# Kernel optimization log

Measured on AMD Instinct MI355X. Metric: run time of the kernel, lower is better.

Reference implementation:

```python
import jax, jax.numpy as jnp
import numpy as np

K_NEIGHBOURS = 2


def setup_inputs() -> dict:
    key = jax.random.key(0)
    k1, k2 = jax.random.split(key)
    train_features = jax.random.normal(k1, (200000, 128), dtype=jnp.float32)
    test_features = jax.random.normal(k2, (2048, 128), dtype=jnp.float32)
    return {"train_features": train_features, "test_features": test_features}


def reference(train_features, test_features):
    # faiss IndexFlatL2 returns SQUARED L2 distances.
    # d2[m, n] = ||q_m||^2 + ||t_n||^2 - 2 q_m . t_n
    q_sq = jnp.sum(test_features * test_features, axis=1, keepdims=True)   # [M, 1]
    t_sq = jnp.sum(train_features * train_features, axis=1)                # [N]
    cross = jnp.einsum('md,nd->mn', test_features, train_features)        # [M, N]
    d2 = q_sq + t_sq[None, :] - 2.0 * cross                               # [M, N]
    # top-2 smallest distances per query -> negate and take top_k
    neg_topk, _ = jax.lax.top_k(-d2, K_NEIGHBOURS)                        # [M, 2]
    # sum of the 2 nearest-neighbour squared distances
    return jnp.sum(-neg_topk, axis=1)                                     # [M]
```

## Files before the change

### kernel.cpp

```cpp
#include <hip/hip_runtime.h>
#include <hip/hip_bf16.h>


typedef short bf16x8 __attribute__((ext_vector_type(8)));
typedef float f32x4 __attribute__((ext_vector_type(4)));

#define N_TRAIN 200000
#define M_QUERY 2048
#define DIMS 128
#define NCH 125
#define PPC (N_TRAIN / NCH)
#define ITERS (PPC / 16)

__device__ __forceinline__ unsigned int bf_bits(float f) {
  unsigned int u = __float_as_uint(f);
  return (u + 0x7FFFu + ((u >> 16) & 1u)) >> 16;
}

__global__ __launch_bounds__(256) void convert_kernel(
    const float* __restrict__ src, unsigned short* __restrict__ dst,
    float* __restrict__ sq, int nrows, float scale) {
  int gtid = blockIdx.x * 256 + threadIdx.x;
  int row = gtid >> 3, sub = gtid & 7;
  if (row >= nrows) return;
  const float4* s4 = reinterpret_cast<const float4*>(src + (size_t)row * DIMS + sub * 16);
  unsigned int pk[8];
  float acc = 0.f;
#pragma unroll
  for (int i = 0; i < 4; ++i) {
    float4 v = s4[i];
    acc += v.x * v.x + v.y * v.y + v.z * v.z + v.w * v.w;
    pk[i * 2 + 0] = bf_bits(v.x * scale) | (bf_bits(v.y * scale) << 16);
    pk[i * 2 + 1] = bf_bits(v.z * scale) | (bf_bits(v.w * scale) << 16);
  }
  uint4* d4 = reinterpret_cast<uint4*>(dst + (size_t)row * DIMS + sub * 16);
  d4[0] = make_uint4(pk[0], pk[1], pk[2], pk[3]);
  d4[1] = make_uint4(pk[4], pk[5], pk[6], pk[7]);
  acc += __shfl_xor(acc, 1);
  acc += __shfl_xor(acc, 2);
  acc += __shfl_xor(acc, 4);
  if (sub == 0) sq[row] = acc;
}

__global__ __launch_bounds__(256) void knn_main(
    const unsigned short* __restrict__ tb, const unsigned short* __restrict__ qb16,
    const float* __restrict__ tsq, float* __restrict__ partials) {
  const int b = blockIdx.x;
  const int g = (b & 7) * NCH + (b >> 3);
  const int chunk = g >> 3;
  const int qblock = (g & 7) << 8;
  const int tid = threadIdx.x;
  const int w = tid >> 6, l = tid & 63;
  const int lo = l & 15, hi = l >> 4;
  const int qw = qblock + w * 64;

  __shared__ char smem[4][2 * 4096];
  char* lbase = smem[w];

  bf16x8 a[4][4];
#pragma unroll
  for (int t = 0; t < 4; ++t)
#pragma unroll
    for (int kf = 0; kf < 4; ++kf)
      a[t][kf] = *reinterpret_cast<const bf16x8*>(
          qb16 + (size_t)(qw + t * 16 + lo) * DIMS + kf * 32 + hi * 8);

  const int offE = hi * 256 + ((lo ^ hi) << 4);
  const int offO = (4 + hi) * 256 + ((lo ^ (4 + hi)) << 4);
  const char* gt = reinterpret_cast<const char*>(tb) + (size_t)chunk * PPC * 256;
  const float* tq = tsq + chunk * PPC;

  int roff[4];
#pragma unroll
  for (int kf = 0; kf < 4; ++kf)
    roff[kf] = lo * 256 + ((((kf << 2) + hi) ^ (lo & 7)) << 4);

  const float INF = __builtin_inff();
  float best1[4][4], best2[4][4];
#pragma unroll
  for (int t = 0; t < 4; ++t)
#pragma unroll
    for (int r = 0; r < 4; ++r) { best1[t][r] = INF; best2[t][r] = INF; }

#define ISSUE(T, BUF, TV)                                                      \
  do {                                                                         \
    const char* _s = gt + (size_t)(T) * 4096;                                  \
    char* _d = lbase + (BUF) * 4096;                                           \
    __builtin_amdgcn_global_load_lds(                                          \
        (const __attribute__((address_space(1))) void*)(_s + offE),            \
        (__attribute__((address_space(3))) void*)_d, 16, 0, 0);                \
    __builtin_amdgcn_global_load_lds(                                          \
        (const __attribute__((address_space(1))) void*)(_s + offO),            \
        (__attribute__((address_space(3))) void*)(_d + 1024), 16, 0, 0);       \
    __builtin_amdgcn_global_load_lds(                                          \
        (const __attribute__((address_space(1))) void*)(_s + 2048 + offE),     \
        (__attribute__((address_space(3))) void*)(_d + 2048), 16, 0, 0);       \
    __builtin_amdgcn_global_load_lds(                                          \
        (const __attribute__((address_space(1))) void*)(_s + 2048 + offO),     \
        (__attribute__((address_space(3))) void*)(_d + 3072), 16, 0, 0);       \
    TV = tq[(T) * 16 + lo];                                                    \
  } while (0)

#define READF(F, BUF)                                                          \
  do {                                                                         \
    const char* _buf = lbase + (BUF) * 4096;                                   \
    F[0] = *reinterpret_cast<const bf16x8*>(_buf + roff[0]);                   \
    F[1] = *reinterpret_cast<const bf16x8*>(_buf + roff[1]);                   \
    F[2] = *reinterpret_cast<const bf16x8*>(_buf + roff[2]);                   \
    F[3] = *reinterpret_cast<const bf16x8*>(_buf + roff[3]);                   \
  } while (0)

#define MFMA_TOP2(F, TV)                                                       \
  do {                                                                         \
    f32x4 c = {TV, TV, TV, TV};                                                \
    __builtin_amdgcn_s_setprio(1);                                             \
    _Pragma("unroll")                                                          \
    for (int t = 0; t < 4; ++t) {                                              \
      f32x4 acc = __builtin_amdgcn_mfma_f32_16x16x32_bf16(a[t][0], F[0], c, 0, 0, 0); \
      acc = __builtin_amdgcn_mfma_f32_16x16x32_bf16(a[t][1], F[1], acc, 0, 0, 0);     \
      acc = __builtin_amdgcn_mfma_f32_16x16x32_bf16(a[t][2], F[2], acc, 0, 0, 0);     \
      acc = __builtin_amdgcn_mfma_f32_16x16x32_bf16(a[t][3], F[3], acc, 0, 0, 0);     \
      _Pragma("unroll")                                                        \
      for (int r = 0; r < 4; ++r) {                                            \
        float s0 = acc[r];             \
        float n1 = fminf(best1[t][r], s0);                                     \
        float n2 = __builtin_amdgcn_fmed3f(best1[t][r], best2[t][r], s0);      \
        best1[t][r] = n1;                                                      \
        best2[t][r] = n2;                                                      \
      }                                                                        \
    }                                                                          \
    __builtin_amdgcn_s_setprio(0);                                             \
  } while (0)

  bf16x8 fA[4], fB[4];
  float tvA, tvB;
  ISSUE(0, 0, tvA);
  ISSUE(1, 1, tvB);
  asm volatile("s_waitcnt vmcnt(5)" ::: "memory");
  READF(fA, 0);

  for (int it = 0; it + 3 < ITERS; it += 2) {
    {
      float t0 = tvA;
      asm volatile("s_waitcnt lgkmcnt(0)" ::: "memory");
      ISSUE(it + 2, 0, tvA);
      asm volatile("s_waitcnt vmcnt(5)" ::: "memory");
      READF(fB, 1);
      MFMA_TOP2(fA, t0);
    }
    {
      float t1 = tvB;
      asm volatile("s_waitcnt lgkmcnt(0)" ::: "memory");
      ISSUE(it + 3, 1, tvB);
      asm volatile("s_waitcnt vmcnt(5)" ::: "memory");
      READF(fA, 0);
      MFMA_TOP2(fB, t1);
    }
  }
  {
    float t0 = tvA;
    asm volatile("s_waitcnt vmcnt(0)" ::: "memory");
    READF(fB, 1);
    MFMA_TOP2(fA, t0);
    MFMA_TOP2(fB, tvB);
  }

#undef ISSUE
#undef READF
#undef MFMA_TOP2

#pragma unroll
  for (int t = 0; t < 4; ++t)
#pragma unroll
    for (int r = 0; r < 4; ++r) {
      float v1 = best1[t][r], v2 = best2[t][r];
#pragma unroll
      for (int m = 1; m < 16; m <<= 1) {
        float o1 = __shfl_xor(v1, m);
        float o2 = __shfl_xor(v2, m);
        float n1 = fminf(v1, o1);
        float n2 = fminf(fmaxf(v1, o1), fminf(v2, o2));
        v1 = n1;
        v2 = n2;
      }
      best1[t][r] = v1;
      best2[t][r] = v2;
    }
  if (lo == 0) {
#pragma unroll
    for (int t = 0; t < 4; ++t)
#pragma unroll
      for (int r = 0; r < 4; ++r) {
        int q = qw + t * 16 + hi * 4 + r;
        float* p = partials + ((size_t)chunk * M_QUERY + q) * 2;
        p[0] = best1[t][r];
        p[1] = best2[t][r];
      }
  }
}

__global__ __launch_bounds__(256) void knn_reduce(
    const float* __restrict__ partials, const float* __restrict__ qsq,
    float* __restrict__ out, int nchunk) {
  int q = blockIdx.x * 256 + threadIdx.x;
  if (q >= M_QUERY) return;
  const float INF = __builtin_inff();
  float b1 = INF, b2 = INF;
  for (int c = 0; c < nchunk; ++c) {
    const float* p = partials + ((size_t)c * M_QUERY + q) * 2;
    float v = p[0];
    float n1 = fminf(b1, v);
    float n2 = __builtin_amdgcn_fmed3f(b1, b2, v);
    b1 = n1; b2 = n2;
    v = p[1];
    n1 = fminf(b1, v);
    n2 = __builtin_amdgcn_fmed3f(b1, b2, v);
    b1 = n1; b2 = n2;
  }
  out[q] = 2.f * qsq[q] + b1 + b2;
}

extern "C" void kernel_launch(void* const* d_in, const int* in_sizes, int n_in,
                              void* d_out, int out_size, void* d_ws, size_t ws_size,
                              hipStream_t stream) {
  const float* train = (const float*)d_in[0];
  const float* test  = (const float*)d_in[1];
  float* out = (float*)d_out;
  char* ws = (char*)d_ws;

  size_t off_tb  = 0;
  size_t off_qb  = off_tb  + (size_t)N_TRAIN * DIMS * 2;
  size_t off_tsq = off_qb  + (size_t)M_QUERY * DIMS * 2;
  size_t off_qsq = off_tsq + (size_t)N_TRAIN * 4;
  size_t off_pt  = off_qsq + (size_t)M_QUERY * 4;
  size_t need125 = off_pt + (size_t)NCH * M_QUERY * 2 * 4;
  if (ws_size < need125) return;

  unsigned short* tbp = (unsigned short*)(ws + off_tb);
  unsigned short* qb  = (unsigned short*)(ws + off_qb);
  float* tsq = (float*)(ws + off_tsq);
  float* qsq = (float*)(ws + off_qsq);
  float* part = (float*)(ws + off_pt);

  hipLaunchKernelGGL(convert_kernel, dim3((N_TRAIN * 8) / 256), dim3(256), 0, stream,
                     train, tbp, tsq, N_TRAIN, 1.0f);
  hipLaunchKernelGGL(convert_kernel, dim3((M_QUERY * 8) / 256), dim3(256), 0, stream,
                     test, qb, qsq, M_QUERY, -2.0f);
  hipLaunchKernelGGL(knn_main, dim3(NCH * 8), dim3(256), 0, stream,
                     tbp, qb, tsq, part);
  hipLaunchKernelGGL(knn_reduce, dim3(M_QUERY / 256), dim3(256), 0, stream,
                     part, qsq, out, NCH);
}
```

Before: 203.0 us.

## Deepen train-tile pipeline to four LDS buffers and stage train norms in LDS

Replaces the two-buffer ping-pong with a four-slot ring that keeps three global-to-LDS tile loads in flight, so each wave waits less on memory latency before its MFMAs. The per-chunk train squared norms (6.4 KB) are preloaded into shared memory once, behind a block barrier, instead of being fetched from global memory on every iteration. A sched_barrier pins the order of loads and MFMAs. LDS use grows to about 70 KB per block, which can lower occupancy. The vmcnt(8) waits before reads of ring slots that the next issue overwrites also need to be correct.

```diff
diff --git a/kernel.cpp b/kernel.cpp
--- a/kernel.cpp
+++ b/kernel.cpp
@@ -54,7 +54,8 @@
   const int lo = l & 15, hi = l >> 4;
   const int qw = qblock + w * 64;
 
-  __shared__ char smem[4][2 * 4096];
+  __shared__ float tsq_s[PPC];
+  __shared__ char smem[4][4 * 4096];
   char* lbase = smem[w];
 
   bf16x8 a[4][4];
@@ -65,10 +66,11 @@
       a[t][kf] = *reinterpret_cast<const bf16x8*>(
           qb16 + (size_t)(qw + t * 16 + lo) * DIMS + kf * 32 + hi * 8);
 
+  for (int i = tid; i < PPC; i += 256) tsq_s[i] = tsq[chunk * PPC + i];
+
   const int offE = hi * 256 + ((lo ^ hi) << 4);
   const int offO = (4 + hi) * 256 + ((lo ^ (4 + hi)) << 4);
   const char* gt = reinterpret_cast<const char*>(tb) + (size_t)chunk * PPC * 256;
-  const float* tq = tsq + chunk * PPC;
 
   int roff[4];
 #pragma unroll
@@ -82,32 +84,29 @@
 #pragma unroll
     for (int r = 0; r < 4; ++r) { best1[t][r] = INF; best2[t][r] = INF; }
 
-#define ISSUE(T, BUF, TV)                                                      \
+#define ISSUE(T, BP)                                                           \
   do {                                                                         \
     const char* _s = gt + (size_t)(T) * 4096;                                  \
-    char* _d = lbase + (BUF) * 4096;                                           \
     __builtin_amdgcn_global_load_lds(                                          \
         (const __attribute__((address_space(1))) void*)(_s + offE),            \
-        (__attribute__((address_space(3))) void*)_d, 16, 0, 0);                \
+        (__attribute__((address_space(3))) void*)(BP), 16, 0, 0);              \
     __builtin_amdgcn_global_load_lds(                                          \
         (const __attribute__((address_space(1))) void*)(_s + offO),            \
-        (__attribute__((address_space(3))) void*)(_d + 1024), 16, 0, 0);       \
+        (__attribute__((address_space(3))) void*)((BP) + 1024), 16, 0, 0);     \
     __builtin_amdgcn_global_load_lds(                                          \
         (const __attribute__((address_space(1))) void*)(_s + 2048 + offE),     \
-        (__attribute__((address_space(3))) void*)(_d + 2048), 16, 0, 0);       \
+        (__attribute__((address_space(3))) void*)((BP) + 2048), 16, 0, 0);     \
     __builtin_amdgcn_global_load_lds(                                          \
         (const __attribute__((address_space(1))) void*)(_s + 2048 + offO),     \
-        (__attribute__((address_space(3))) void*)(_d + 3072), 16, 0, 0);       \
-    TV = tq[(T) * 16 + lo];                                                    \
+        (__attribute__((address_space(3))) void*)((BP) + 3072), 16, 0, 0);     \
   } while (0)
 
-#define READF(F, BUF)                                                          \
+#define READF(F, BP)                                                           \
   do {                                                                         \
-    const char* _buf = lbase + (BUF) * 4096;                                   \
-    F[0] = *reinterpret_cast<const bf16x8*>(_buf + roff[0]);                   \
-    F[1] = *reinterpret_cast<const bf16x8*>(_buf + roff[1]);                   \
-    F[2] = *reinterpret_cast<const bf16x8*>(_buf + roff[2]);                   \
-    F[3] = *reinterpret_cast<const bf16x8*>(_buf + roff[3]);                   \
+    F[0] = *reinterpret_cast<const bf16x8*>((BP) + roff[0]);                   \
+    F[1] = *reinterpret_cast<const bf16x8*>((BP) + roff[1]);                   \
+    F[2] = *reinterpret_cast<const bf16x8*>((BP) + roff[2]);                   \
+    F[3] = *reinterpret_cast<const bf16x8*>((BP) + roff[3]);                   \
   } while (0)
 
 #define MFMA_TOP2(F, TV)                                                       \
@@ -132,37 +131,38 @@
     __builtin_amdgcn_s_setprio(0);                                             \
   } while (0)
 
-  bf16x8 fA[4], fB[4];
-  float tvA, tvB;
-  ISSUE(0, 0, tvA);
-  ISSUE(1, 1, tvB);
-  asm volatile("s_waitcnt vmcnt(5)" ::: "memory");
-  READF(fA, 0);
-
-  for (int it = 0; it + 3 < ITERS; it += 2) {
-    {
-      float t0 = tvA;
-      asm volatile("s_waitcnt lgkmcnt(0)" ::: "memory");
-      ISSUE(it + 2, 0, tvA);
-      asm volatile("s_waitcnt vmcnt(5)" ::: "memory");
-      READF(fB, 1);
-      MFMA_TOP2(fA, t0);
-    }
-    {
-      float t1 = tvB;
-      asm volatile("s_waitcnt lgkmcnt(0)" ::: "memory");
-      ISSUE(it + 3, 1, tvB);
-      asm volatile("s_waitcnt vmcnt(5)" ::: "memory");
-      READF(fA, 0);
-      MFMA_TOP2(fB, t1);
-    }
+  __syncthreads();
+
+  ISSUE(0, lbase);
+  ISSUE(1, lbase + 4096);
+  ISSUE(2, lbase + 8192);
+
+  bf16x8 f[4];
+  for (int it = 0; it < ITERS - 3; ++it) {
+    asm volatile("s_waitcnt vmcnt(8)" ::: "memory");
+    char* bp = lbase + ((it & 3) << 12);
+    READF(f, bp);
+    float tv = tsq_s[it * 16 + lo];
+    ISSUE(it + 3, lbase + (((it + 3) & 3) << 12));
+    __builtin_amdgcn_sched_barrier(0);
+    MFMA_TOP2(f, tv);
   }
   {
-    float t0 = tvA;
+    asm volatile("s_waitcnt vmcnt(8)" ::: "memory");
+    char* bp = lbase + (((ITERS - 3) & 3) << 12);
+    READF(f, bp);
+    float tv = tsq_s[(ITERS - 3) * 16 + lo];
+    MFMA_TOP2(f, tv);
+    asm volatile("s_waitcnt vmcnt(4)" ::: "memory");
+    bp = lbase + (((ITERS - 2) & 3) << 12);
+    READF(f, bp);
+    tv = tsq_s[(ITERS - 2) * 16 + lo];
+    MFMA_TOP2(f, tv);
     asm volatile("s_waitcnt vmcnt(0)" ::: "memory");
-    READF(fB, 1);
-    MFMA_TOP2(fA, t0);
-    MFMA_TOP2(fB, tvB);
+    bp = lbase + (((ITERS - 1) & 3) << 12);
+    READF(f, bp);
+    tv = tsq_s[(ITERS - 1) * 16 + lo];
+    MFMA_TOP2(f, tv);
   }
 
 #undef ISSUE
```

Result: slower. 214.5 us (+5.6%).
